# Kernel tuning notes

Hardware: AMD Instinct MI355X
Metric: run time of the kernel (lower is better)

The kernel has to match this reference:

```python
import jax, jax.numpy as jnp
import numpy as np

B, S, IN_DIM, EMBED, HEADS, WINDOW = 2, 2048, 1024, 1024, 16, 256
HEAD_DIM = EMBED // HEADS
NEG_FILL = -9.0e15


def setup_inputs() -> dict:
    key = jax.random.key(0)
    k1, k2, k3, k4 = jax.random.split(key, 4)
    x = jax.random.normal(k1, (B, S, IN_DIM), dtype=jnp.float32)
    # padding_mask: positions with value 1 get zeroed in q/k/v (matches masked_fill semantics)
    padding_mask = jax.random.randint(k2, (B, S), 0, 2, dtype=jnp.int32)
    # xavier-uniform-like init scale for the linear weights
    lim_qkv = np.sqrt(6.0 / (IN_DIM + 3 * EMBED)).astype(np.float32)
    lim_o = np.sqrt(6.0 / (EMBED + EMBED)).astype(np.float32)
    Wqkv = jax.random.uniform(k3, (3 * EMBED, IN_DIM), jnp.float32, -lim_qkv, lim_qkv)
    bqkv = jnp.zeros((3 * EMBED,), jnp.float32)
    Wo = jax.random.uniform(k4, (EMBED, EMBED), jnp.float32, -lim_o, lim_o)
    bo = jnp.zeros((EMBED,), jnp.float32)
    return {"x": x, "padding_mask": padding_mask, "Wqkv": Wqkv, "bqkv": bqkv, "Wo": Wo, "bo": bo}


def reference(x, padding_mask, Wqkv, bqkv, Wo, bo):
    b, s, _ = x.shape
    h, hd, pad = HEADS, HEAD_DIM, WINDOW // 2
    # qkv projection: torch Linear is x @ W.T + b
    qkv = x @ Wqkv.T + bqkv                      # [B, S, 3E]
    qkv = qkv.reshape(b, s, h, 3 * hd).transpose(0, 2, 1, 3)  # [B, H, S, 3*hd]
    q, k, v = jnp.split(qkv, 3, axis=-1)          # each [B, H, S, hd]
    # zero out padded positions in q, k, v where padding_mask == 1
    pm = (padding_mask != 0)[:, None, :, None]    # [B, 1, S, 1]
    q = jnp.where(pm, 0.0, q)
    k = jnp.where(pm, 0.0, k)
    v = jnp.where(pm, 0.0, v)
    # dense banded scores: identical math to the unfold-based band compute
    scores = jnp.einsum("bhsd,bhtd->bhst", q, k)  # [B, H, S, S]
    idx = jnp.arange(s)
    band = jnp.abs(idx[None, :] - idx[:, None]) <= pad  # |i-j| <= window/2
    scores = jnp.where(band, scores, jnp.float32(NEG_FILL))
    scores = scores / jnp.sqrt(jnp.float32(hd))   # original scales AFTER the fill
    attn = jax.nn.softmax(scores, axis=-1)        # [B, H, S, S]
    vals = jnp.einsum("bhst,bhtd->bhsd", attn, v)  # [B, H, S, hd]
    vals = vals.transpose(0, 2, 1, 3).reshape(b, s, h * hd)  # [B, S, E]
    return vals @ Wo.T + bo
```

## Files before the change

kernel.cpp:

```cpp
#include <hip/hip_runtime.h>
#include <stdint.h>

#define S_LEN 2048
#define EMBED 1024
#define HEADS 16
#define HD 64
#define M_ROWS 4096
#define N_QKV 3072
#define KDIM 1024
#define SP 2336
#define CLP2 200

typedef __attribute__((ext_vector_type(8))) short short8;
typedef __attribute__((ext_vector_type(4))) float f32x4;

__device__ __forceinline__ unsigned short f2bf(float f) {
  union { float f; uint32_t u; } c; c.f = f;
  uint32_t u = c.u;
  u += 0x7fffu + ((u >> 16) & 1u);
  return (unsigned short)(u >> 16);
}

__device__ __forceinline__ void gload_lds16(const unsigned short* g, unsigned short* l) {
  __builtin_amdgcn_global_load_lds(
      (const __attribute__((address_space(1))) void*)g,
      (__attribute__((address_space(3))) void*)l, 16, 0, 0);
}

#define XQ 1048576
#define WQKVQ 786432
#define WOQ 262144
#define CVTQ (XQ + WQKVQ + WOQ)
__global__ __launch_bounds__(256) void cvt3_kernel(
    const float* __restrict__ x, const float* __restrict__ wqkv, const float* __restrict__ wo,
    unsigned short* __restrict__ xb, unsigned short* __restrict__ wqkvb, unsigned short* __restrict__ wob,
    unsigned short* __restrict__ vTp) {
  int i = blockIdx.x * blockDim.x + threadIdx.x;
  if (i < CVTQ) {
    const float* s; unsigned short* d; int off;
    if (i < XQ)               { s = x;    d = xb;    off = i; }
    else if (i < XQ + WQKVQ)  { s = wqkv; d = wqkvb; off = i - XQ; }
    else                      { s = wo;   d = wob;   off = i - XQ - WQKVQ; }
    float4 f = reinterpret_cast<const float4*>(s)[off];
    ushort4 o;
    o.x = f2bf(f.x); o.y = f2bf(f.y); o.z = f2bf(f.z); o.w = f2bf(f.w);
    reinterpret_cast<ushort4*>(d)[off] = o;
  } else {
    int j = i - CVTQ;
    int row = j / 72, p = j % 72;
    int off = row * 584 + (p < 32 ? p : 544 + (p - 32));
    reinterpret_cast<ushort4*>(vTp)[off] = (ushort4){0, 0, 0, 0};
  }
}

__global__ __launch_bounds__(512, 2) void gemm_qkv(
    const unsigned short* __restrict__ A, const unsigned short* __restrict__ Bm,
    const float* __restrict__ bias, const int* __restrict__ pm,
    unsigned short* __restrict__ qo, unsigned short* __restrict__ ko,
    unsigned short* __restrict__ vTp)
{
  __shared__ __align__(16) unsigned short smem[57344];
  const int t = threadIdx.x, wave = t >> 6, lane = t & 63;
  const int m16 = lane & 15, q4 = lane >> 4;
  const int wm = wave >> 1, wn = wave & 1;
  const int bid = blockIdx.x;
  const int mb = bid >> 4, nb = bid & 15;
  const int lrow = lane >> 3;
  const int lsegsw = ((lane & 7) ^ lrow) * 8;
  const unsigned short* gsrc[7];
#pragma unroll
  for (int j = 0; j < 7; j++) {
    int u = wave * 7 + j;
    gsrc[j] = (u < 32 ? A  + (size_t)(mb * 256 + u * 8 + lrow) * KDIM
                      : Bm + (size_t)(nb * 192 + (u - 32) * 8 + lrow) * KDIM)
              + lsegsw;
  }
  const int rsw = (m16 & 7) * 8;

  f32x4 acc[4][6];
#pragma unroll
  for (int i_ = 0; i_ < 4; i_++)
#pragma unroll
    for (int j_ = 0; j_ < 6; j_++) acc[i_][j_] = (f32x4){0.f, 0.f, 0.f, 0.f};

  auto LDA = [&](short8* af, const unsigned short* As, int h) {
#pragma unroll
    for (int mt = 0; mt < 4; mt++)
      af[mt] = *reinterpret_cast<const short8*>(
          &As[(wm * 64 + mt * 16 + m16) * 64 + (((h * 4 + q4) * 8) ^ rsw)]);
  };
  auto LDB3 = [&](short8* bf, const unsigned short* Bs, int h, int n0) {
#pragma unroll
    for (int nt = 0; nt < 3; nt++)
      bf[nt] = *reinterpret_cast<const short8*>(
          &Bs[(wn * 96 + (n0 + nt) * 16 + m16) * 64 + (((h * 4 + q4) * 8) ^ rsw)]);
  };
  auto MM3 = [&](short8* af, short8* bf, int n0) {
#pragma unroll
    for (int mt = 0; mt < 4; mt++)
#pragma unroll
      for (int nt = 0; nt < 3; nt++)
        acc[mt][n0 + nt] =
            __builtin_amdgcn_mfma_f32_16x16x32_bf16(af[mt], bf[nt], acc[mt][n0 + nt], 0, 0, 0);
  };

#pragma unroll
  for (int j = 0; j < 7; j++)
    gload_lds16(gsrc[j], smem + (wave * 7 + j) * 512);
  __builtin_amdgcn_sched_barrier(0);

  for (int T = 0; T < 16; ++T) {
    const int c = T & 1;
    const unsigned short* As = smem + c * 28672;
    const unsigned short* Bs = As + 16384;
    unsigned short* nslab = smem + (c ^ 1) * 28672;
    const int nkt = (T + 1) * 64;
    const bool st = (T < 15);
    short8 af[4], bf[3];

    if (st) {
#pragma unroll
      for (int j = 0; j < 3; j++)
        gload_lds16(gsrc[j] + nkt, nslab + (wave * 7 + j) * 512);
    }
    __builtin_amdgcn_sched_barrier(0);
    if (st) asm volatile("s_waitcnt vmcnt(3)" ::: "memory");
    else    asm volatile("s_waitcnt vmcnt(0)" ::: "memory");
    __builtin_amdgcn_sched_barrier(0);
    __builtin_amdgcn_s_barrier();
    __builtin_amdgcn_sched_barrier(0);
    LDA(af, As, 0);
    LDB3(bf, Bs, 0, 0);
    asm volatile("s_waitcnt lgkmcnt(0)" ::: "memory");
    __builtin_amdgcn_sched_barrier(0);
    __builtin_amdgcn_s_setprio(1);
    MM3(af, bf, 0);
    __builtin_amdgcn_s_setprio(0);
    __builtin_amdgcn_sched_barrier(0);
    __builtin_amdgcn_s_barrier();
    __builtin_amdgcn_sched_barrier(0);

    LDB3(bf, Bs, 0, 3);
    if (st) {
#pragma unroll
      for (int j = 3; j < 5; j++)
        gload_lds16(gsrc[j] + nkt, nslab + (wave * 7 + j) * 512);
    }
    __builtin_amdgcn_sched_barrier(0);
    __builtin_amdgcn_s_barrier();
    asm volatile("s_waitcnt lgkmcnt(0)" ::: "memory");
    __builtin_amdgcn_sched_barrier(0);
    __builtin_amdgcn_s_setprio(1);
    MM3(af, bf, 3);
    __builtin_amdgcn_s_setprio(0);
    __builtin_amdgcn_sched_barrier(0);
    __builtin_amdgcn_s_barrier();
    __builtin_amdgcn_sched_barrier(0);

    LDA(af, As, 1);
    LDB3(bf, Bs, 1, 0);
    if (st) {
#pragma unroll
      for (int j = 5; j < 7; j++)
        gload_lds16(gsrc[j] + nkt, nslab + (wave * 7 + j) * 512);
    }
    __builtin_amdgcn_sched_barrier(0);
    __builtin_amdgcn_s_barrier();
    asm volatile("s_waitcnt lgkmcnt(0)" ::: "memory");
    __builtin_amdgcn_sched_barrier(0);
    __builtin_amdgcn_s_setprio(1);
    MM3(af, bf, 0);
    __builtin_amdgcn_s_setprio(0);
    __builtin_amdgcn_sched_barrier(0);
    __builtin_amdgcn_s_barrier();
    __builtin_amdgcn_sched_barrier(0);

    LDB3(bf, Bs, 1, 3);
    __builtin_amdgcn_sched_barrier(0);
    __builtin_amdgcn_s_barrier();
    asm volatile("s_waitcnt lgkmcnt(0)" ::: "memory");
    __builtin_amdgcn_sched_barrier(0);
    __builtin_amdgcn_s_setprio(1);
    MM3(af, bf, 3);
    __builtin_amdgcn_s_setprio(0);
    __builtin_amdgcn_sched_barrier(0);
    __builtin_amdgcn_s_barrier();
    __builtin_amdgcn_sched_barrier(0);
  }

  float pmv[4][4];
#pragma unroll
  for (int mt = 0; mt < 4; mt++)
#pragma unroll
    for (int reg = 0; reg < 4; reg++) {
      int row = mb * 256 + wm * 64 + mt * 16 + q4 * 4 + reg;
      pmv[mt][reg] = (pm[row] != 0) ? 0.0f : 1.0f;
    }
#pragma unroll
  for (int nt = 0; nt < 6; nt++) {
    int cloc = wn * 96 + nt * 16 + m16;
    float bv = bias[nb * 192 + cloc];
#pragma unroll
    for (int mt = 0; mt < 4; mt++) {
#pragma unroll
      for (int reg = 0; reg < 4; reg++) {
        int rloc = wm * 64 + mt * 16 + q4 * 4 + reg;
        smem[rloc * CLP2 + cloc] = f2bf((acc[mt][nt][reg] + bv) * pmv[mt][reg]);
      }
    }
  }
  __syncthreads();
  const int s0 = mb * 256;
  const int bh = (s0 >> 11) * 16 + nb, s0l = s0 & 2047;
  {
    int r = t >> 1, half = t & 1;
    const unsigned short* sq = &smem[r * CLP2 + half * 32];
    unsigned short* dq = qo + ((size_t)(bh * 2048 + s0l + r)) * 64 + half * 32;
#pragma unroll
    for (int j = 0; j < 4; j++)
      *reinterpret_cast<short8*>(dq + j * 8) = *reinterpret_cast<const short8*>(sq + j * 8);
    const unsigned short* sk = &smem[r * CLP2 + 64 + half * 32];
    unsigned short* dk = ko + ((size_t)(bh * 2048 + s0l + r)) * 64 + half * 32;
#pragma unroll
    for (int j = 0; j < 4; j++)
      *reinterpret_cast<short8*>(dk + j * 8) = *reinterpret_cast<const short8*>(sk + j * 8);
  }
  {
    int d = t & 63, oct = t >> 6;
    unsigned short* dst = vTp + (size_t)(bh * 64 + d) * SP + 128 + s0l + oct * 32;
#pragma unroll
    for (int j8 = 0; j8 < 4; j8++) {
      short8 tmp;
#pragma unroll
      for (int jj = 0; jj < 8; jj++)
        tmp[jj] = (short)smem[(oct * 32 + j8 * 8 + jj) * CLP2 + 128 + d];
      *reinterpret_cast<short8*>(dst + j8 * 8) = tmp;
    }
  }
}

__global__ __launch_bounds__(256) void gemm_out(
    const unsigned short* __restrict__ A, const unsigned short* __restrict__ Bm,
    const float* __restrict__ bias, float* __restrict__ out)
{
  __shared__ __align__(16) unsigned char smemraw[67584];
  unsigned short* smem = (unsigned short*)smemraw;
  float* Cldf = (float*)smemraw;
  const int t = threadIdx.x, wave = t >> 6, lane = t & 63;
  const int m16 = lane & 15, q4 = lane >> 4;
  const int wm = wave >> 1, wn = wave & 1;
  const int bid = blockIdx.x;
  const int nb = bid & 7;
  const int mb = bid >> 3;
  const int lrow = lane >> 3;
  const int lsegsw = ((lane & 7) ^ lrow) * 8;
  const unsigned short* gsrc[8];
#pragma unroll
  for (int j = 0; j < 8; j++) {
    int u = wave * 8 + j;
    gsrc[j] = (u < 16 ? A  + (size_t)(mb * 128 + u * 8 + lrow) * KDIM
                      : Bm + (size_t)(nb * 128 + (u - 16) * 8 + lrow) * KDIM)
              + lsegsw;
  }
  const int rsw = (m16 & 7) * 8;

  f32x4 acc[4][4];
#pragma unroll
  for (int i_ = 0; i_ < 4; i_++)
#pragma unroll
    for (int j_ = 0; j_ < 4; j_++) acc[i_][j_] = (f32x4){0.f, 0.f, 0.f, 0.f};

#pragma unroll
  for (int j = 0; j < 8; j++)
    gload_lds16(gsrc[j], smem + (wave * 8 + j) * 512);
  __builtin_amdgcn_sched_barrier(0);

  for (int T = 0; T < 16; ++T) {
    const int c = T & 1;
    const unsigned short* As = smem + c * 16384;
    const unsigned short* Bs = As + 8192;
    unsigned short* nslab = smem + (c ^ 1) * 16384;
    const int nkt = (T + 1) * 64;
    const bool st = (T < 15);

    if (st) {
#pragma unroll
      for (int j = 0; j < 8; j++)
        gload_lds16(gsrc[j] + nkt, nslab + (wave * 8 + j) * 512);
    }
    __builtin_amdgcn_sched_barrier(0);
    if (st) asm volatile("s_waitcnt vmcnt(8)" ::: "memory");
    else    asm volatile("s_waitcnt vmcnt(0)" ::: "memory");
    __builtin_amdgcn_sched_barrier(0);
    __builtin_amdgcn_s_barrier();
    __builtin_amdgcn_sched_barrier(0);
#pragma unroll
    for (int h = 0; h < 2; h++) {
      short8 af[4], bf[4];
#pragma unroll
      for (int mt = 0; mt < 4; mt++)
        af[mt] = *reinterpret_cast<const short8*>(
            &As[(wm * 64 + mt * 16 + m16) * 64 + (((h * 4 + q4) * 8) ^ rsw)]);
#pragma unroll
      for (int nt = 0; nt < 4; nt++)
        bf[nt] = *reinterpret_cast<const short8*>(
            &Bs[(wn * 64 + nt * 16 + m16) * 64 + (((h * 4 + q4) * 8) ^ rsw)]);
      asm volatile("s_waitcnt lgkmcnt(0)" ::: "memory");
      __builtin_amdgcn_sched_barrier(0);
      __builtin_amdgcn_s_setprio(1);
#pragma unroll
      for (int mt = 0; mt < 4; mt++)
#pragma unroll
        for (int nt = 0; nt < 4; nt++)
          acc[mt][nt] = __builtin_amdgcn_mfma_f32_16x16x32_bf16(af[mt], bf[nt], acc[mt][nt], 0, 0, 0);
      __builtin_amdgcn_s_setprio(0);
      __builtin_amdgcn_sched_barrier(0);
    }
    __builtin_amdgcn_sched_barrier(0);
    __builtin_amdgcn_s_barrier();
    __builtin_amdgcn_sched_barrier(0);
  }

#pragma unroll
  for (int nt = 0; nt < 4; nt++) {
    int cloc = wn * 64 + nt * 16 + m16;
    float bv = bias[nb * 128 + cloc];
#pragma unroll
    for (int mt = 0; mt < 4; mt++) {
#pragma unroll
      for (int reg = 0; reg < 4; reg++) {
        int rloc = wm * 64 + mt * 16 + q4 * 4 + reg;
        Cldf[rloc * 132 + cloc] = acc[mt][nt][reg] + bv;
      }
    }
  }
  __syncthreads();
  {
    int r = t >> 1, half = t & 1;
    float* dst = out + (size_t)(mb * 128 + r) * EMBED + nb * 128 + half * 64;
    const float* srcl = &Cldf[r * 132 + half * 64];
#pragma unroll
    for (int j = 0; j < 16; j++)
      *reinterpret_cast<float4*>(dst + j * 4) = *reinterpret_cast<const float4*>(srcl + j * 4);
  }
}

__global__ __launch_bounds__(256, 2) void attn_kernel(
    const unsigned short* __restrict__ q, const unsigned short* __restrict__ k,
    const unsigned short* __restrict__ vTp, unsigned short* __restrict__ vals)
{
  __shared__ __align__(16) unsigned short smem[40960];
  unsigned short* Ks = smem;
  unsigned short* Vs = smem + 20480;
  unsigned short* Pld = smem;

  const int bid = blockIdx.x;
  const int bh = bid & 31, qg = bid >> 5;
  const int lane = threadIdx.x & 63, wave = threadIdx.x >> 6;
  const int i0b = qg * 64;
  const int i0 = i0b + wave * 16;
  const int m16 = lane & 15, q4 = lane >> 4;

  const unsigned short* qb = q + ((size_t)(bh * 2048 + i0 + m16)) * 64 + q4 * 8;
  short8 aq0 = *reinterpret_cast<const short8*>(qb);
  short8 aq1 = *reinterpret_cast<const short8*>(qb + 32);
  __builtin_amdgcn_sched_barrier(0);

  const unsigned short* kbase = k + (size_t)bh * 2048 * 64;
#pragma unroll
  for (int n = 0; n < 10; n++) {
    int idx = (n * 4 + wave) * 64 + lane;
    int krow = idx >> 3, seg = idx & 7;
    int grow = i0b - 128 + krow;
    grow = grow < 0 ? 0 : (grow > 2047 ? 2047 : grow);
    int lseg = seg ^ (krow & 7);
    gload_lds16(kbase + (size_t)grow * 64 + lseg * 8, Ks + (n * 4 + wave) * 512);
  }
  __builtin_amdgcn_sched_barrier(0);
  const unsigned short* vbase = vTp + (size_t)bh * 64 * SP + i0b;
#pragma unroll
  for (int n = 0; n < 10; n++) {
    int idx = (n * 4 + wave) * 64 + lane;
    int vrow = idx / 40, rem = idx % 40;
    int l = (rem & ~7) | ((rem & 7) ^ (vrow & 7));
    gload_lds16(vbase + (size_t)vrow * SP + l * 8, Vs + (n * 4 + wave) * 512);
  }
  __builtin_amdgcn_sched_barrier(0);

  asm volatile("s_waitcnt vmcnt(10)" ::: "memory");
  __builtin_amdgcn_sched_barrier(0);
  __builtin_amdgcn_s_barrier();
  __builtin_amdgcn_sched_barrier(0);

  float sum[4] = {0.f, 0.f, 0.f, 0.f};
  uint32_t pP[18][2];
#pragma unroll
  for (int ct = 0; ct < 18; ct++) {
    int r = (wave + ct) * 16 + m16;
    int js = i0b - 128 + r;
    const unsigned short* kr = Ks + r * 64;
    short8 b0 = *reinterpret_cast<const short8*>(kr + ((q4 ^ (r & 7)) * 8));
    short8 b1 = *reinterpret_cast<const short8*>(kr + (((q4 + 4) ^ (r & 7)) * 8));
    f32x4 a = {0.f, 0.f, 0.f, 0.f};
    a = __builtin_amdgcn_mfma_f32_16x16x32_bf16(aq0, b0, a, 0, 0, 0);
    a = __builtin_amdgcn_mfma_f32_16x16x32_bf16(aq1, b1, a, 0, 0, 0);
    unsigned short pe[4];
#pragma unroll
    for (int reg = 0; reg < 4; reg++) {
      int i = i0 + q4 * 4 + reg;
      bool valid = (js >= 0) && (js < 2048) && (js >= i - 128) && (js <= i + 128);
      float e = valid ? __expf(a[reg] * 0.125f) : 0.0f;
      sum[reg] += e;
      pe[reg] = f2bf(e);
    }
    pP[ct][0] = (uint32_t)pe[0] | ((uint32_t)pe[1] << 16);
    pP[ct][1] = (uint32_t)pe[2] | ((uint32_t)pe[3] << 16);
  }
  float rden[4];
#pragma unroll
  for (int reg = 0; reg < 4; reg++) {
    float s = sum[reg];
    s += __shfl_xor(s, 1);
    s += __shfl_xor(s, 2);
    s += __shfl_xor(s, 4);
    s += __shfl_xor(s, 8);
    rden[reg] = 1.0f / s;
  }

  __syncthreads();

  unsigned short* Pw = Pld + wave * 16 * 296;
#pragma unroll
  for (int ct = 0; ct < 18; ct++) {
    Pw[(q4 * 4 + 0) * 296 + ct * 16 + m16] = (unsigned short)(pP[ct][0] & 0xFFFF);
    Pw[(q4 * 4 + 1) * 296 + ct * 16 + m16] = (unsigned short)(pP[ct][0] >> 16);
    Pw[(q4 * 4 + 2) * 296 + ct * 16 + m16] = (unsigned short)(pP[ct][1] & 0xFFFF);
    Pw[(q4 * 4 + 3) * 296 + ct * 16 + m16] = (unsigned short)(pP[ct][1] >> 16);
  }
  short8 ap[9];
#pragma unroll
  for (int kc = 0; kc < 9; kc++)
    ap[kc] = *reinterpret_cast<const short8*>(&Pw[m16 * 296 + kc * 32 + q4 * 8]);

  const int b = bh >> 4, h = bh & 15;
#pragma unroll
  for (int dt = 0; dt < 4; dt++) {
    int vrow = dt * 16 + m16;
    const unsigned short* vr = Vs + vrow * 320;
    f32x4 av = {0.f, 0.f, 0.f, 0.f};
#pragma unroll
    for (int kc = 0; kc < 9; kc++) {
      int jseg = kc * 4 + wave * 2 + q4;
      if (jseg > 39) jseg = 39;
      int sseg = (jseg & ~7) | ((jseg & 7) ^ (vrow & 7));
      short8 bv = *reinterpret_cast<const short8*>(vr + sseg * 8);
      av = __builtin_amdgcn_mfma_f32_16x16x32_bf16(ap[kc], bv, av, 0, 0, 0);
    }
#pragma unroll
    for (int reg = 0; reg < 4; reg++)
      Pw[(q4 * 4 + reg) * 296 + dt * 16 + m16] = f2bf(av[reg] * rden[reg]);
  }
  {
    int srow = lane >> 2, seg = lane & 3;
    unsigned short* dst = vals + ((size_t)(b * 2048 + i0 + srow)) * 1024 + h * 64 + seg * 16;
    const unsigned short* srcl = &Pw[srow * 296 + seg * 16];
    *reinterpret_cast<short8*>(dst)     = *reinterpret_cast<const short8*>(srcl);
    *reinterpret_cast<short8*>(dst + 8) = *reinterpret_cast<const short8*>(srcl + 8);
  }
}

extern "C" void kernel_launch(void* const* d_in, const int* in_sizes, int n_in,
                              void* d_out, int out_size, void* d_ws, size_t ws_size,
                              hipStream_t stream) {
  const float* x    = (const float*)d_in[0];
  const int*   pm   = (const int*)d_in[1];
  const float* Wqkv = (const float*)d_in[2];
  const float* bqkv = (const float*)d_in[3];
  const float* Wo   = (const float*)d_in[4];
  const float* bo   = (const float*)d_in[5];
  float* out = (float*)d_out;
  char* ws = (char*)d_ws;

  unsigned short* xb    = (unsigned short*)(ws);
  unsigned short* vals  = (unsigned short*)(ws);
  unsigned short* Wqkvb = (unsigned short*)(ws +  8388608);
  unsigned short* Wob   = (unsigned short*)(ws + 14680064);
  unsigned short* qbuf  = (unsigned short*)(ws + 16777216);
  unsigned short* kbuf  = (unsigned short*)(ws + 25165824);
  unsigned short* vTp   = (unsigned short*)(ws + 33554432);

  cvt3_kernel<<<8768, 256, 0, stream>>>(x, Wqkv, Wo, xb, Wqkvb, Wob, vTp);
  gemm_qkv<<<256, 512, 0, stream>>>(xb, Wqkvb, bqkv, pm, qbuf, kbuf, vTp);
  attn_kernel<<<1024, 256, 0, stream>>>(qbuf, kbuf, vTp, vals);
  gemm_out<<<256, 256, 0, stream>>>(vals, Wob, bo, out);
}
```

Before: 159.3 us.

## Shrink QKV GEMM tile to 128 rows with 256 threads and simplify pipeline

Halves the M tile of the QKV projection GEMM from 256 to 128 rows, running 4-wave blocks over twice as many workgroups. The interleaved four-phase schedule, which split the global-to-LDS prefetch across sub-steps, is replaced by issuing the whole next-tile prefetch up front. Each K tile is then computed in two half-steps, each loading 4 A and 6 B fragments before its MFMAs. The aim is more blocks per GPU and simpler synchronisation, at the cost of less operand reuse per block and more total global traffic for the weight matrix.

```diff
diff --git a/kernel.cpp b/kernel.cpp
--- a/kernel.cpp
+++ b/kernel.cpp
@@ -53,13 +53,13 @@
   }
 }
 
-__global__ __launch_bounds__(512, 2) void gemm_qkv(
+__global__ __launch_bounds__(256) void gemm_qkv(
     const unsigned short* __restrict__ A, const unsigned short* __restrict__ Bm,
     const float* __restrict__ bias, const int* __restrict__ pm,
     unsigned short* __restrict__ qo, unsigned short* __restrict__ ko,
     unsigned short* __restrict__ vTp)
 {
-  __shared__ __align__(16) unsigned short smem[57344];
+  __shared__ __align__(16) unsigned short smem[40960];
   const int t = threadIdx.x, wave = t >> 6, lane = t & 63;
   const int m16 = lane & 15, q4 = lane >> 4;
   const int wm = wave >> 1, wn = wave & 1;
@@ -67,12 +67,12 @@
   const int mb = bid >> 4, nb = bid & 15;
   const int lrow = lane >> 3;
   const int lsegsw = ((lane & 7) ^ lrow) * 8;
-  const unsigned short* gsrc[7];
-#pragma unroll
-  for (int j = 0; j < 7; j++) {
-    int u = wave * 7 + j;
-    gsrc[j] = (u < 32 ? A  + (size_t)(mb * 256 + u * 8 + lrow) * KDIM
-                      : Bm + (size_t)(nb * 192 + (u - 32) * 8 + lrow) * KDIM)
+  const unsigned short* gsrc[10];
+#pragma unroll
+  for (int j = 0; j < 10; j++) {
+    int u = wave * 10 + j;
+    gsrc[j] = (u < 16 ? A  + (size_t)(mb * 128 + u * 8 + lrow) * KDIM
+                      : Bm + (size_t)(nb * 192 + (u - 16) * 8 + lrow) * KDIM)
               + lsegsw;
   }
   const int rsw = (m16 & 7) * 8;
@@ -83,109 +83,55 @@
 #pragma unroll
     for (int j_ = 0; j_ < 6; j_++) acc[i_][j_] = (f32x4){0.f, 0.f, 0.f, 0.f};
 
-  auto LDA = [&](short8* af, const unsigned short* As, int h) {
-#pragma unroll
-    for (int mt = 0; mt < 4; mt++)
-      af[mt] = *reinterpret_cast<const short8*>(
-          &As[(wm * 64 + mt * 16 + m16) * 64 + (((h * 4 + q4) * 8) ^ rsw)]);
-  };
-  auto LDB3 = [&](short8* bf, const unsigned short* Bs, int h, int n0) {
-#pragma unroll
-    for (int nt = 0; nt < 3; nt++)
-      bf[nt] = *reinterpret_cast<const short8*>(
-          &Bs[(wn * 96 + (n0 + nt) * 16 + m16) * 64 + (((h * 4 + q4) * 8) ^ rsw)]);
-  };
-  auto MM3 = [&](short8* af, short8* bf, int n0) {
-#pragma unroll
-    for (int mt = 0; mt < 4; mt++)
-#pragma unroll
-      for (int nt = 0; nt < 3; nt++)
-        acc[mt][n0 + nt] =
-            __builtin_amdgcn_mfma_f32_16x16x32_bf16(af[mt], bf[nt], acc[mt][n0 + nt], 0, 0, 0);
-  };
-
-#pragma unroll
-  for (int j = 0; j < 7; j++)
-    gload_lds16(gsrc[j], smem + (wave * 7 + j) * 512);
+#pragma unroll
+  for (int j = 0; j < 10; j++)
+    gload_lds16(gsrc[j], smem + (wave * 10 + j) * 512);
   __builtin_amdgcn_sched_barrier(0);
 
   for (int T = 0; T < 16; ++T) {
     const int c = T & 1;
-    const unsigned short* As = smem + c * 28672;
-    const unsigned short* Bs = As + 16384;
-    unsigned short* nslab = smem + (c ^ 1) * 28672;
+    const unsigned short* As = smem + c * 20480;
+    const unsigned short* Bs = As + 8192;
+    unsigned short* nslab = smem + (c ^ 1) * 20480;
     const int nkt = (T + 1) * 64;
     const bool st = (T < 15);
-    short8 af[4], bf[3];
 
     if (st) {
 #pragma unroll
-      for (int j = 0; j < 3; j++)
-        gload_lds16(gsrc[j] + nkt, nslab + (wave * 7 + j) * 512);
-    }
-    __builtin_amdgcn_sched_barrier(0);
-    if (st) asm volatile("s_waitcnt vmcnt(3)" ::: "memory");
+      for (int j = 0; j < 10; j++)
+        gload_lds16(gsrc[j] + nkt, nslab + (wave * 10 + j) * 512);
+    }
+    __builtin_amdgcn_sched_barrier(0);
+    if (st) asm volatile("s_waitcnt vmcnt(10)" ::: "memory");
     else    asm volatile("s_waitcnt vmcnt(0)" ::: "memory");
     __builtin_amdgcn_sched_barrier(0);
     __builtin_amdgcn_s_barrier();
     __builtin_amdgcn_sched_barrier(0);
-    LDA(af, As, 0);
-    LDB3(bf, Bs, 0, 0);
-    asm volatile("s_waitcnt lgkmcnt(0)" ::: "memory");
-    __builtin_amdgcn_sched_barrier(0);
-    __builtin_amdgcn_s_setprio(1);
-    MM3(af, bf, 0);
-    __builtin_amdgcn_s_setprio(0);
+#pragma unroll
+    for (int h = 0; h < 2; h++) {
+      short8 af[4], bf[6];
+#pragma unroll
+      for (int mt = 0; mt < 4; mt++)
+        af[mt] = *reinterpret_cast<const short8*>(
+            &As[(wm * 64 + mt * 16 + m16) * 64 + (((h * 4 + q4) * 8) ^ rsw)]);
+#pragma unroll
+      for (int nt = 0; nt < 6; nt++)
+        bf[nt] = *reinterpret_cast<const short8*>(
+            &Bs[(wn * 96 + nt * 16 + m16) * 64 + (((h * 4 + q4) * 8) ^ rsw)]);
+      asm volatile("s_waitcnt lgkmcnt(0)" ::: "memory");
+      __builtin_amdgcn_sched_barrier(0);
+      __builtin_amdgcn_s_setprio(1);
+#pragma unroll
+      for (int mt = 0; mt < 4; mt++)
+#pragma unroll
+        for (int nt = 0; nt < 6; nt++)
+          acc[mt][nt] = __builtin_amdgcn_mfma_f32_16x16x32_bf16(af[mt], bf[nt], acc[mt][nt], 0, 0, 0);
+      __builtin_amdgcn_s_setprio(0);
+      __builtin_amdgcn_sched_barrier(0);
+    }
     __builtin_amdgcn_sched_barrier(0);
     __builtin_amdgcn_s_barrier();
     __builtin_amdgcn_sched_barrier(0);
-
-    LDB3(bf, Bs, 0, 3);
-    if (st) {
-#pragma unroll
-      for (int j = 3; j < 5; j++)
-        gload_lds16(gsrc[j] + nkt, nslab + (wave * 7 + j) * 512);
-    }
-    __builtin_amdgcn_sched_barrier(0);
-    __builtin_amdgcn_s_barrier();
-    asm volatile("s_waitcnt lgkmcnt(0)" ::: "memory");
-    __builtin_amdgcn_sched_barrier(0);
-    __builtin_amdgcn_s_setprio(1);
-    MM3(af, bf, 3);
-    __builtin_amdgcn_s_setprio(0);
-    __builtin_amdgcn_sched_barrier(0);
-    __builtin_amdgcn_s_barrier();
-    __builtin_amdgcn_sched_barrier(0);
-
-    LDA(af, As, 1);
-    LDB3(bf, Bs, 1, 0);
-    if (st) {
-#pragma unroll
-      for (int j = 5; j < 7; j++)
-        gload_lds16(gsrc[j] + nkt, nslab + (wave * 7 + j) * 512);
-    }
-    __builtin_amdgcn_sched_barrier(0);
-    __builtin_amdgcn_s_barrier();
-    asm volatile("s_waitcnt lgkmcnt(0)" ::: "memory");
-    __builtin_amdgcn_sched_barrier(0);
-    __builtin_amdgcn_s_setprio(1);
-    MM3(af, bf, 0);
-    __builtin_amdgcn_s_setprio(0);
-    __builtin_amdgcn_sched_barrier(0);
-    __builtin_amdgcn_s_barrier();
-    __builtin_amdgcn_sched_barrier(0);
-
-    LDB3(bf, Bs, 1, 3);
-    __builtin_amdgcn_sched_barrier(0);
-    __builtin_amdgcn_s_barrier();
-    asm volatile("s_waitcnt lgkmcnt(0)" ::: "memory");
-    __builtin_amdgcn_sched_barrier(0);
-    __builtin_amdgcn_s_setprio(1);
-    MM3(af, bf, 3);
-    __builtin_amdgcn_s_setprio(0);
-    __builtin_amdgcn_sched_barrier(0);
-    __builtin_amdgcn_s_barrier();
-    __builtin_amdgcn_sched_barrier(0);
   }
 
   float pmv[4][4];
@@ -193,7 +139,7 @@
   for (int mt = 0; mt < 4; mt++)
 #pragma unroll
     for (int reg = 0; reg < 4; reg++) {
-      int row = mb * 256 + wm * 64 + mt * 16 + q4 * 4 + reg;
+      int row = mb * 128 + wm * 64 + mt * 16 + q4 * 4 + reg;
       pmv[mt][reg] = (pm[row] != 0) ? 0.0f : 1.0f;
     }
 #pragma unroll
@@ -210,7 +156,7 @@
     }
   }
   __syncthreads();
-  const int s0 = mb * 256;
+  const int s0 = mb * 128;
   const int bh = (s0 >> 11) * 16 + nb, s0l = s0 & 2047;
   {
     int r = t >> 1, half = t & 1;
@@ -226,14 +172,14 @@
       *reinterpret_cast<short8*>(dk + j * 8) = *reinterpret_cast<const short8*>(sk + j * 8);
   }
   {
-    int d = t & 63, oct = t >> 6;
-    unsigned short* dst = vTp + (size_t)(bh * 64 + d) * SP + 128 + s0l + oct * 32;
+    int d = t & 63, qtr = t >> 6;
+    unsigned short* dst = vTp + (size_t)(bh * 64 + d) * SP + 128 + s0l + qtr * 32;
 #pragma unroll
     for (int j8 = 0; j8 < 4; j8++) {
       short8 tmp;
 #pragma unroll
       for (int jj = 0; jj < 8; jj++)
-        tmp[jj] = (short)smem[(oct * 32 + j8 * 8 + jj) * CLP2 + 128 + d];
+        tmp[jj] = (short)smem[(qtr * 32 + j8 * 8 + jj) * CLP2 + 128 + d];
       *reinterpret_cast<short8*>(dst + j8 * 8) = tmp;
     }
   }
@@ -490,7 +436,7 @@
   unsigned short* vTp   = (unsigned short*)(ws + 33554432);
 
   cvt3_kernel<<<8768, 256, 0, stream>>>(x, Wqkv, Wo, xb, Wqkvb, Wob, vTp);
-  gemm_qkv<<<256, 512, 0, stream>>>(xb, Wqkvb, bqkv, pm, qbuf, kbuf, vTp);
+  gemm_qkv<<<512, 256, 0, stream>>>(xb, Wqkvb, bqkv, pm, qbuf, kbuf, vTp);
   attn_kernel<<<1024, 256, 0, stream>>>(qbuf, kbuf, vTp, vals);
   gemm_out<<<256, 256, 0, stream>>>(vals, Wob, bo, out);
 }
```

Measured after the change: 159.1 us. About the same (-0.1%).
